# Performance work log

Hardware: AMD Instinct MI355X
Metric: run time of the kernel (lower is better)

Reference implementation:

```python
import jax, jax.numpy as jnp
import numpy as np

B, D, H, W = 8, 512, 96, 96
K1, K2, K3 = 16, 32, 64
EPS = 1e-5


def setup_inputs() -> dict:
    key = jax.random.key(0)
    ks = jax.random.split(key, 20)
    std1 = 1.0 / np.sqrt(K1 * D)
    std2 = 1.0 / np.sqrt(K2 * D)
    std3 = 1.0 / np.sqrt(K3 * D)
    return {
        "X": jax.random.normal(ks[0], (B, D, H, W), jnp.float32),
        "W1": jax.random.normal(ks[1], (D, D), jnp.float32) * 0.02,
        "bn1_scale": jax.random.uniform(ks[2], (D,), jnp.float32, 0.5, 1.5),
        "bn1_bias": jax.random.normal(ks[3], (D,), jnp.float32) * 0.1,
        "bn1_mean": jax.random.normal(ks[4], (D,), jnp.float32) * 0.1,
        "bn1_var": jax.random.uniform(ks[5], (D,), jnp.float32, 0.5, 1.5),
        "W2": jax.random.normal(ks[6], (D, D), jnp.float32) * 0.02,
        "bn2_scale": jax.random.uniform(ks[7], (D,), jnp.float32, 0.5, 1.5),
        "bn2_bias": jax.random.normal(ks[8], (D,), jnp.float32) * 0.1,
        "bn2_mean": jax.random.normal(ks[9], (D,), jnp.float32) * 0.1,
        "bn2_var": jax.random.uniform(ks[10], (D,), jnp.float32, 0.5, 1.5),
        "cw1": jax.random.uniform(ks[11], (D, K1), jnp.float32, -std1, std1),
        "cw2": jax.random.uniform(ks[12], (D, K2), jnp.float32, -std2, std2),
        "cw3": jax.random.uniform(ks[13], (D, K3), jnp.float32, -std3, std3),
        "gamma1": jax.random.normal(ks[14], (1,), jnp.float32) * 0.1,
        "gamma2": jax.random.normal(ks[15], (1,), jnp.float32) * 0.1,
        "gamma3": jax.random.normal(ks[16], (1,), jnp.float32) * 0.1,
    }


def _conv_bn_relu(x, w, s, b, m, v):
    # 1x1 conv (no bias) + eval-mode BatchNorm + ReLU; x: [B,D,H,W], w: [Dout,Din]
    y = jnp.einsum('bdhw,ed->behw', x, w)
    scale = (s / jnp.sqrt(v + EPS))[None, :, None, None]
    shift = (b - m * s / jnp.sqrt(v + EPS))[None, :, None, None]
    return jax.nn.relu(y * scale + shift)


def _soft_vq(x, cw, gamma):
    # x: [B,D,H,W], cw: [D,K] -> gamma * softmax(Xt@cw) @ cw^T, reshaped back
    b, d, h, w = x.shape
    xt = x.reshape(b, d, h * w).transpose(0, 2, 1)          # [B,N,D]
    a = jax.nn.softmax(jnp.einsum('bnd,dk->bnk', xt, cw), axis=-1)
    e = jnp.einsum('bnk,dk->bnd', a, cw)                    # [B,N,D]
    return gamma[0] * e.transpose(0, 2, 1).reshape(b, d, h, w)


def reference(X, W1, bn1_scale, bn1_bias, bn1_mean, bn1_var,
              W2, bn2_scale, bn2_bias, bn2_mean, bn2_var,
              cw1, cw2, cw3, gamma1, gamma2, gamma3):
    X2 = _conv_bn_relu(X, W1, bn1_scale, bn1_bias, bn1_mean, bn1_var)
    X3 = _conv_bn_relu(X2, W2, bn2_scale, bn2_bias, bn2_mean, bn2_var)
    E1 = _soft_vq(X, cw1, gamma1)
    E2 = _soft_vq(X2, cw2, gamma2)
    E3 = _soft_vq(X3, cw3, gamma3)
    return X + E1 + E2 + E3
```

## Files before the change

kernel.cpp:

```cpp
#include <hip/hip_runtime.h>
#include <hip/hip_bf16.h>
#include <stdint.h>

#define DD 512
#define HW 9216
#define NBATCH 8
#define BN_EPS 1e-5f

typedef __attribute__((ext_vector_type(8))) short short8;
typedef __attribute__((ext_vector_type(4))) float f32x4;

__device__ __forceinline__ unsigned short f2bf(float f) {
  union { float f; uint32_t u; } v; v.f = f;
  uint32_t r = v.u + 0x7FFFu + ((v.u >> 16) & 1u);
  return (unsigned short)(r >> 16);
}

__global__ void prep_kernel(const float* __restrict__ W1, const float* __restrict__ W2,
                            const float* __restrict__ s1, const float* __restrict__ b1,
                            const float* __restrict__ m1, const float* __restrict__ v1,
                            const float* __restrict__ s2, const float* __restrict__ b2,
                            const float* __restrict__ m2, const float* __restrict__ v2,
                            unsigned short* __restrict__ W1b, unsigned short* __restrict__ W2b,
                            float* __restrict__ sc1, float* __restrict__ sh1,
                            float* __restrict__ sc2, float* __restrict__ sh2) {
  int t = blockIdx.x * 256 + threadIdx.x;
  if (t < DD * DD) { W1b[t] = f2bf(W1[t]); W2b[t] = f2bf(W2[t]); }
  if (t < DD) {
    float a = s1[t] * rsqrtf(v1[t] + BN_EPS);
    sc1[t] = a; sh1[t] = b1[t] - m1[t] * a;
    float c = s2[t] * rsqrtf(v2[t] + BN_EPS);
    sc2[t] = c; sh2[t] = b2[t] - m2[t] * c;
  }
}

__global__ void prep_cw(const float* __restrict__ cw1, const float* __restrict__ cw2,
                        const float* __restrict__ cw3,
                        unsigned short* __restrict__ CWt, unsigned short* __restrict__ CWc) {
  int t = blockIdx.x * 256 + threadIdx.x;
  int d = t >> 7, k = t & 127;
  float v = 0.f;
  if (k < 16) v = cw1[d * 16 + k];
  else if (k < 48) v = cw2[d * 32 + (k - 16)];
  else if (k < 112) v = cw3[d * 64 + (k - 48)];
  unsigned short bv = f2bf(v);
  CWc[d * 128 + k] = bv;
  if (k < 112) CWt[k * 512 + d] = bv;
}

template <int TIN_BF16>
__global__ __launch_bounds__(256) void gemm_bn(
    const void* __restrict__ Xin_, const unsigned short* __restrict__ Wb,
    const float* __restrict__ scale, const float* __restrict__ shift,
    unsigned short* __restrict__ Yout) {
  const int b  = blockIdx.z;
  const int e0 = blockIdx.y * 128;
  const int n0 = blockIdx.x * 128;
  const int tid  = threadIdx.x;
  const int lane = tid & 63;
  const int wave = tid >> 6;
  const int wr = wave >> 1, wc = wave & 1;

  __shared__ __align__(16) unsigned short Alds[128 * 32];
  __shared__ __align__(16) unsigned short Blds[128 * 40];

  const float* Xf          = (const float*)Xin_ + (size_t)b * DD * HW;
  const unsigned short* Xh = (const unsigned short*)Xin_ + (size_t)b * DD * HW;

  f32x4 acc[4][4];
#pragma unroll
  for (int i = 0; i < 4; i++)
#pragma unroll
    for (int j = 0; j < 4; j++) acc[i][j] = (f32x4)0.0f;

  const int arow  = tid >> 1;
  const int ahalf = tid & 1;
  const int bcol  = tid & 127;
  const int bdh   = tid >> 7;

  const int koff = (lane >> 4) * 8;
  const int lrow = lane & 15;

  for (int kt = 0; kt < DD / 32; ++kt) {
    const int d0 = kt * 32;
    __syncthreads();
    {
      const unsigned short* src = Wb + (size_t)(e0 + arow) * DD + d0 + ahalf * 16;
      short8 v0 = *(const short8*)(src);
      short8 v1 = *(const short8*)(src + 8);
      *(short8*)&Alds[arow * 32 + ahalf * 16]     = v0;
      *(short8*)&Alds[arow * 32 + ahalf * 16 + 8] = v1;
    }
    {
      unsigned short* dst = &Blds[bcol * 40 + bdh * 16];
      if (TIN_BF16) {
        const unsigned short* src = Xh + (size_t)(d0 + bdh * 16) * HW + n0 + bcol;
#pragma unroll
        for (int j = 0; j < 8; j++) {
          uint32_t u0 = src[(size_t)(2 * j) * HW];
          uint32_t u1 = src[(size_t)(2 * j + 1) * HW];
          *(uint32_t*)&dst[2 * j] = u0 | (u1 << 16);
        }
      } else {
        const float* src = Xf + (size_t)(d0 + bdh * 16) * HW + n0 + bcol;
#pragma unroll
        for (int j = 0; j < 8; j++) {
          uint32_t u0 = f2bf(src[(size_t)(2 * j) * HW]);
          uint32_t u1 = f2bf(src[(size_t)(2 * j + 1) * HW]);
          *(uint32_t*)&dst[2 * j] = u0 | (u1 << 16);
        }
      }
    }
    __syncthreads();

    short8 af[4], bfr[4];
#pragma unroll
    for (int ma = 0; ma < 4; ma++)
      af[ma] = *(const short8*)&Alds[(wr * 64 + ma * 16 + lrow) * 32 + koff];
#pragma unroll
    for (int nb = 0; nb < 4; nb++)
      bfr[nb] = *(const short8*)&Blds[(wc * 64 + nb * 16 + lrow) * 40 + koff];
#pragma unroll
    for (int ma = 0; ma < 4; ma++)
#pragma unroll
      for (int nb = 0; nb < 4; nb++)
        acc[ma][nb] = __builtin_amdgcn_mfma_f32_16x16x32_bf16(af[ma], bfr[nb], acc[ma][nb], 0, 0, 0);
  }

  const int rbase = (lane >> 4) * 4;
  const int col   = lane & 15;
#pragma unroll
  for (int ma = 0; ma < 4; ma++) {
    const int ebase = e0 + wr * 64 + ma * 16 + rbase;
    float sc[4], sh[4];
#pragma unroll
    for (int r = 0; r < 4; r++) { sc[r] = scale[ebase + r]; sh[r] = shift[ebase + r]; }
#pragma unroll
    for (int nb = 0; nb < 4; nb++) {
      const int n = n0 + wc * 64 + nb * 16 + col;
      const size_t base = (size_t)b * DD * HW + (size_t)ebase * HW + n;
#pragma unroll
      for (int r = 0; r < 4; r++) {
        float y = acc[ma][nb][r] * sc[r] + sh[r];
        y = y > 0.f ? y : 0.f;
        Yout[base + (size_t)r * HW] = f2bf(y);
      }
    }
  }
}

__global__ __launch_bounds__(256) void vq_mfma(
    const float* __restrict__ X, const unsigned short* __restrict__ X2,
    const unsigned short* __restrict__ X3,
    const unsigned short* __restrict__ CWt,
    const unsigned short* __restrict__ CWc,
    const float* __restrict__ gg1, const float* __restrict__ gg2,
    const float* __restrict__ gg3, float* __restrict__ out) {
  const int b  = blockIdx.y;
  const int n0 = blockIdx.x * 64;
  const int tid  = threadIdx.x;
  const int lane = tid & 63;
  const int wv   = tid >> 6;
  const int hi = lane >> 4, lr = lane & 15;

  __shared__ __align__(16) unsigned short Pl[64 * 136];
  __shared__ __align__(16) unsigned short Stg[17408];

  const size_t bbase = (size_t)b * DD * HW;

  f32x4 accl[7];
#pragma unroll
  for (int t = 0; t < 7; t++) accl[t] = (f32x4)0.0f;

  const int sn = tid & 63;
  const int sg = tid >> 6;

  for (int kt = 0; kt < 16; ++kt) {
    const int d0 = kt * 32;
    __syncthreads();
    {
      const float* src = X + bbase + (size_t)(d0 + sg * 8) * HW + n0 + sn;
      unsigned short* dst = &Stg[sn * 40 + sg * 8];
#pragma unroll
      for (int j = 0; j < 4; j++) {
        uint32_t u0 = f2bf(src[(size_t)(2 * j) * HW]);
        uint32_t u1 = f2bf(src[(size_t)(2 * j + 1) * HW]);
        *(uint32_t*)&dst[2 * j] = u0 | (u1 << 16);
      }
    }
    {
      const unsigned short* src = X2 + bbase + (size_t)(d0 + sg * 8) * HW + n0 + sn;
      unsigned short* dst = &Stg[2560 + sn * 40 + sg * 8];
#pragma unroll
      for (int j = 0; j < 4; j++) {
        uint32_t u0 = src[(size_t)(2 * j) * HW];
        uint32_t u1 = src[(size_t)(2 * j + 1) * HW];
        *(uint32_t*)&dst[2 * j] = u0 | (u1 << 16);
      }
    }
    {
      const unsigned short* src = X3 + bbase + (size_t)(d0 + sg * 8) * HW + n0 + sn;
      unsigned short* dst = &Stg[5120 + sn * 40 + sg * 8];
#pragma unroll
      for (int j = 0; j < 4; j++) {
        uint32_t u0 = src[(size_t)(2 * j) * HW];
        uint32_t u1 = src[(size_t)(2 * j + 1) * HW];
        *(uint32_t*)&dst[2 * j] = u0 | (u1 << 16);
      }
    }
    {
#pragma unroll
      for (int u = tid; u < 1792; u += 256) {
        int row = u >> 4, c = u & 15;
        uint32_t v = *(const uint32_t*)&CWt[row * 512 + d0 + c * 2];
        *(uint32_t*)&Stg[7680 + row * 40 + c * 2] = v;
      }
    }
    __syncthreads();

    short8 a0 = *(const short8*)&Stg[(wv * 16 + lr) * 40 + hi * 8];
    short8 a1 = *(const short8*)&Stg[2560 + (wv * 16 + lr) * 40 + hi * 8];
    short8 a2 = *(const short8*)&Stg[5120 + (wv * 16 + lr) * 40 + hi * 8];
    short8 bt[7];
#pragma unroll
    for (int t = 0; t < 7; t++)
      bt[t] = *(const short8*)&Stg[7680 + (t * 16 + lr) * 40 + hi * 8];
    accl[0] = __builtin_amdgcn_mfma_f32_16x16x32_bf16(a0, bt[0], accl[0], 0, 0, 0);
    accl[1] = __builtin_amdgcn_mfma_f32_16x16x32_bf16(a1, bt[1], accl[1], 0, 0, 0);
    accl[2] = __builtin_amdgcn_mfma_f32_16x16x32_bf16(a1, bt[2], accl[2], 0, 0, 0);
#pragma unroll
    for (int t = 3; t < 7; t++)
      accl[t] = __builtin_amdgcn_mfma_f32_16x16x32_bf16(a2, bt[t], accl[t], 0, 0, 0);
  }

  {
    const float gv1 = gg1[0], gv2 = gg2[0], gv3 = gg3[0];
    float p[7][4];
#pragma unroll
    for (int r = 0; r < 4; ++r) {
      {
        float v = accl[0][r];
        float m = v;
#pragma unroll
        for (int mk = 1; mk <= 8; mk <<= 1) m = fmaxf(m, __shfl_xor(m, mk, 64));
        float e = __expf(v - m);
        float s = e;
#pragma unroll
        for (int mk = 1; mk <= 8; mk <<= 1) s += __shfl_xor(s, mk, 64);
        p[0][r] = e * (gv1 / s);
      }
      {
        float v1 = accl[1][r], v2 = accl[2][r];
        float m = fmaxf(v1, v2);
#pragma unroll
        for (int mk = 1; mk <= 8; mk <<= 1) m = fmaxf(m, __shfl_xor(m, mk, 64));
        float e1 = __expf(v1 - m), e2 = __expf(v2 - m);
        float s = e1 + e2;
#pragma unroll
        for (int mk = 1; mk <= 8; mk <<= 1) s += __shfl_xor(s, mk, 64);
        float sc = gv2 / s;
        p[1][r] = e1 * sc; p[2][r] = e2 * sc;
      }
      {
        float m = fmaxf(fmaxf(accl[3][r], accl[4][r]), fmaxf(accl[5][r], accl[6][r]));
#pragma unroll
        for (int mk = 1; mk <= 8; mk <<= 1) m = fmaxf(m, __shfl_xor(m, mk, 64));
        float e[4], s = 0.f;
#pragma unroll
        for (int t = 0; t < 4; t++) { e[t] = __expf(accl[3 + t][r] - m); s += e[t]; }
#pragma unroll
        for (int mk = 1; mk <= 8; mk <<= 1) s += __shfl_xor(s, mk, 64);
        float sc = gv3 / s;
#pragma unroll
        for (int t = 0; t < 4; t++) p[3 + t][r] = e[t] * sc;
      }
    }
    const int posr = wv * 16 + 4 * hi;
#pragma unroll
    for (int t = 0; t < 7; ++t)
#pragma unroll
      for (int r = 0; r < 4; ++r)
        Pl[(posr + r) * 136 + t * 16 + lr] = f2bf(p[t][r]);
    {
      int pp = tid & 63, cg = tid >> 6;
#pragma unroll
      for (int i = 0; i < 4; ++i) Pl[pp * 136 + 112 + cg * 4 + i] = 0;
    }
  }
  __syncthreads();

  short8 pf[4][4];
#pragma unroll
  for (int ct = 0; ct < 4; ++ct)
#pragma unroll
    for (int s = 0; s < 4; ++s)
      pf[ct][s] = *(const short8*)&Pl[(ct * 16 + lr) * 136 + s * 32 + hi * 8];

  const float* Xg = X + bbase;
  float* outg = out + bbase;
  for (int chunk = 0; chunk < 4; ++chunk) {
    __syncthreads();
    {
      int row = tid >> 1, half = tid & 1;
      const unsigned short* src = CWc + (size_t)(chunk * 128 + row) * 128 + half * 64;
      unsigned short* dst = &Stg[row * 136 + half * 64];
#pragma unroll
      for (int i = 0; i < 8; ++i)
        *(short8*)(dst + i * 8) = *(const short8*)(src + i * 8);
    }
    __syncthreads();
#pragma unroll
    for (int dl = wv; dl < 8; dl += 4) {
      f32x4 acc[4];
#pragma unroll
      for (int ct = 0; ct < 4; ++ct) acc[ct] = (f32x4)0.0f;
#pragma unroll
      for (int s = 0; s < 4; ++s) {
        short8 af = *(const short8*)&Stg[(dl * 16 + lr) * 136 + s * 32 + hi * 8];
#pragma unroll
        for (int ct = 0; ct < 4; ++ct)
          acc[ct] = __builtin_amdgcn_mfma_f32_16x16x32_bf16(af, pf[ct][s], acc[ct], 0, 0, 0);
      }
      const int dgb = chunk * 128 + dl * 16 + 4 * hi;
#pragma unroll
      for (int ct = 0; ct < 4; ++ct) {
        const int n = n0 + ct * 16 + lr;
#pragma unroll
        for (int r = 0; r < 4; ++r) {
          const size_t a = (size_t)(dgb + r) * HW + n;
          outg[a] = Xg[a] + acc[ct][r];
        }
      }
    }
  }
}

extern "C" void kernel_launch(void* const* d_in, const int* in_sizes, int n_in,
                              void* d_out, int out_size, void* d_ws, size_t ws_size,
                              hipStream_t stream) {
  const float* X    = (const float*)d_in[0];
  const float* W1   = (const float*)d_in[1];
  const float* bn1s = (const float*)d_in[2];
  const float* bn1b = (const float*)d_in[3];
  const float* bn1m = (const float*)d_in[4];
  const float* bn1v = (const float*)d_in[5];
  const float* W2   = (const float*)d_in[6];
  const float* bn2s = (const float*)d_in[7];
  const float* bn2b = (const float*)d_in[8];
  const float* bn2m = (const float*)d_in[9];
  const float* bn2v = (const float*)d_in[10];
  const float* cw1  = (const float*)d_in[11];
  const float* cw2  = (const float*)d_in[12];
  const float* cw3  = (const float*)d_in[13];
  const float* g1   = (const float*)d_in[14];
  const float* g2   = (const float*)d_in[15];
  const float* g3   = (const float*)d_in[16];

  char* ws = (char*)d_ws;
  unsigned short* W1b = (unsigned short*)(ws);
  unsigned short* W2b = (unsigned short*)(ws + 524288);
  float* sc1 = (float*)(ws + 1048576);
  float* sh1 = sc1 + 512;
  float* sc2 = sh1 + 512;
  float* sh2 = sc2 + 512;
  unsigned short* CWt = (unsigned short*)(ws + 1064960);
  unsigned short* CWc = (unsigned short*)(ws + 1064960 + 114688);
  unsigned short* X2 = (unsigned short*)(ws + (1 << 21));
  unsigned short* X3 = X2 + (size_t)NBATCH * DD * HW;

  prep_kernel<<<1024, 256, 0, stream>>>(W1, W2, bn1s, bn1b, bn1m, bn1v,
                                        bn2s, bn2b, bn2m, bn2v,
                                        W1b, W2b, sc1, sh1, sc2, sh2);
  prep_cw<<<256, 256, 0, stream>>>(cw1, cw2, cw3, CWt, CWc);

  dim3 gg(HW / 128, DD / 128, NBATCH);
  gemm_bn<0><<<gg, 256, 0, stream>>>((const void*)X,  W1b, sc1, sh1, X2);
  gemm_bn<1><<<gg, 256, 0, stream>>>((const void*)X2, W2b, sc2, sh2, X3);

  dim3 gv(HW / 64, NBATCH);
  vq_mfma<<<gv, 256, 0, stream>>>(X, X2, X3, CWt, CWc, g1, g2, g3, (float*)d_out);
}
```

Baseline: 329.5 us.

## Load VQ operands directly into MFMA registers, drop LDS staging and barriers

The VQ kernel no longer stages X/X2/X3 tiles and codewords through shared memory with two barriers per k-step. Each lane now loads its MFMA operand fragments straight from global memory, with the operand roles swapped so the softmax reduction works along the register dimension and needs fewer cross-lane shuffles. The output projection also reads codewords directly from global memory instead of copying chunks into LDS. This removes synchronisation and LDS traffic, at the cost of more redundant global/L2 reads of the codewords by every wave.

```diff
diff --git a/kernel.cpp b/kernel.cpp
--- a/kernel.cpp
+++ b/kernel.cpp
@@ -9,6 +9,8 @@
 
 typedef __attribute__((ext_vector_type(8))) short short8;
 typedef __attribute__((ext_vector_type(4))) float f32x4;
+
+union bf8u { uint32_t u[4]; short8 v; };
 
 __device__ __forceinline__ unsigned short f2bf(float f) {
   union { float f; uint32_t u; } v; v.f = f;
@@ -164,127 +166,117 @@
   const int hi = lane >> 4, lr = lane & 15;
 
   __shared__ __align__(16) unsigned short Pl[64 * 136];
-  __shared__ __align__(16) unsigned short Stg[17408];
 
   const size_t bbase = (size_t)b * DD * HW;
+  const int myn = n0 + wv * 16 + lr;
+  const float*          pX  = X  + bbase + myn;
+  const unsigned short* pX2 = X2 + bbase + myn;
+  const unsigned short* pX3 = X3 + bbase + myn;
 
   f32x4 accl[7];
 #pragma unroll
   for (int t = 0; t < 7; t++) accl[t] = (f32x4)0.0f;
-
-  const int sn = tid & 63;
-  const int sg = tid >> 6;
 
   for (int kt = 0; kt < 16; ++kt) {
     const int d0 = kt * 32;
-    __syncthreads();
-    {
-      const float* src = X + bbase + (size_t)(d0 + sg * 8) * HW + n0 + sn;
-      unsigned short* dst = &Stg[sn * 40 + sg * 8];
-#pragma unroll
-      for (int j = 0; j < 4; j++) {
-        uint32_t u0 = f2bf(src[(size_t)(2 * j) * HW]);
-        uint32_t u1 = f2bf(src[(size_t)(2 * j + 1) * HW]);
-        *(uint32_t*)&dst[2 * j] = u0 | (u1 << 16);
-      }
-    }
-    {
-      const unsigned short* src = X2 + bbase + (size_t)(d0 + sg * 8) * HW + n0 + sn;
-      unsigned short* dst = &Stg[2560 + sn * 40 + sg * 8];
-#pragma unroll
-      for (int j = 0; j < 4; j++) {
-        uint32_t u0 = src[(size_t)(2 * j) * HW];
-        uint32_t u1 = src[(size_t)(2 * j + 1) * HW];
-        *(uint32_t*)&dst[2 * j] = u0 | (u1 << 16);
-      }
-    }
-    {
-      const unsigned short* src = X3 + bbase + (size_t)(d0 + sg * 8) * HW + n0 + sn;
-      unsigned short* dst = &Stg[5120 + sn * 40 + sg * 8];
-#pragma unroll
-      for (int j = 0; j < 4; j++) {
-        uint32_t u0 = src[(size_t)(2 * j) * HW];
-        uint32_t u1 = src[(size_t)(2 * j + 1) * HW];
-        *(uint32_t*)&dst[2 * j] = u0 | (u1 << 16);
-      }
-    }
-    {
-#pragma unroll
-      for (int u = tid; u < 1792; u += 256) {
-        int row = u >> 4, c = u & 15;
-        uint32_t v = *(const uint32_t*)&CWt[row * 512 + d0 + c * 2];
-        *(uint32_t*)&Stg[7680 + row * 40 + c * 2] = v;
-      }
-    }
-    __syncthreads();
-
-    short8 a0 = *(const short8*)&Stg[(wv * 16 + lr) * 40 + hi * 8];
-    short8 a1 = *(const short8*)&Stg[2560 + (wv * 16 + lr) * 40 + hi * 8];
-    short8 a2 = *(const short8*)&Stg[5120 + (wv * 16 + lr) * 40 + hi * 8];
-    short8 bt[7];
+    const size_t rbase = (size_t)(d0 + hi * 8) * HW;
+
+    bf8u bx, b2, b3;
+#pragma unroll
+    for (int j = 0; j < 4; j++) {
+      uint32_t u0 = f2bf(pX[rbase + (size_t)(2 * j) * HW]);
+      uint32_t u1 = f2bf(pX[rbase + (size_t)(2 * j + 1) * HW]);
+      bx.u[j] = u0 | (u1 << 16);
+    }
+#pragma unroll
+    for (int j = 0; j < 4; j++) {
+      uint32_t u0 = pX2[rbase + (size_t)(2 * j) * HW];
+      uint32_t u1 = pX2[rbase + (size_t)(2 * j + 1) * HW];
+      b2.u[j] = u0 | (u1 << 16);
+    }
+#pragma unroll
+    for (int j = 0; j < 4; j++) {
+      uint32_t u0 = pX3[rbase + (size_t)(2 * j) * HW];
+      uint32_t u1 = pX3[rbase + (size_t)(2 * j + 1) * HW];
+      b3.u[j] = u0 | (u1 << 16);
+    }
+
+    short8 at[7];
 #pragma unroll
     for (int t = 0; t < 7; t++)
-      bt[t] = *(const short8*)&Stg[7680 + (t * 16 + lr) * 40 + hi * 8];
-    accl[0] = __builtin_amdgcn_mfma_f32_16x16x32_bf16(a0, bt[0], accl[0], 0, 0, 0);
-    accl[1] = __builtin_amdgcn_mfma_f32_16x16x32_bf16(a1, bt[1], accl[1], 0, 0, 0);
-    accl[2] = __builtin_amdgcn_mfma_f32_16x16x32_bf16(a1, bt[2], accl[2], 0, 0, 0);
+      at[t] = *(const short8*)&CWt[(size_t)(t * 16 + lr) * 512 + d0 + hi * 8];
+
+    accl[0] = __builtin_amdgcn_mfma_f32_16x16x32_bf16(at[0], bx.v, accl[0], 0, 0, 0);
+    accl[1] = __builtin_amdgcn_mfma_f32_16x16x32_bf16(at[1], b2.v, accl[1], 0, 0, 0);
+    accl[2] = __builtin_amdgcn_mfma_f32_16x16x32_bf16(at[2], b2.v, accl[2], 0, 0, 0);
 #pragma unroll
     for (int t = 3; t < 7; t++)
-      accl[t] = __builtin_amdgcn_mfma_f32_16x16x32_bf16(a2, bt[t], accl[t], 0, 0, 0);
+      accl[t] = __builtin_amdgcn_mfma_f32_16x16x32_bf16(at[t], b3.v, accl[t], 0, 0, 0);
   }
 
   {
     const float gv1 = gg1[0], gv2 = gg2[0], gv3 = gg3[0];
-    float p[7][4];
-#pragma unroll
-    for (int r = 0; r < 4; ++r) {
-      {
-        float v = accl[0][r];
-        float m = v;
-#pragma unroll
-        for (int mk = 1; mk <= 8; mk <<= 1) m = fmaxf(m, __shfl_xor(m, mk, 64));
-        float e = __expf(v - m);
-        float s = e;
-#pragma unroll
-        for (int mk = 1; mk <= 8; mk <<= 1) s += __shfl_xor(s, mk, 64);
-        p[0][r] = e * (gv1 / s);
+    const int prow = (wv * 16 + lr) * 136;
+    {
+      float m = fmaxf(fmaxf(accl[0][0], accl[0][1]), fmaxf(accl[0][2], accl[0][3]));
+      m = fmaxf(m, __shfl_xor(m, 16, 64));
+      m = fmaxf(m, __shfl_xor(m, 32, 64));
+      float e[4], s = 0.f;
+#pragma unroll
+      for (int r = 0; r < 4; r++) { e[r] = __expf(accl[0][r] - m); s += e[r]; }
+      s += __shfl_xor(s, 16, 64);
+      s += __shfl_xor(s, 32, 64);
+      float sc = gv1 / s;
+#pragma unroll
+      for (int r = 0; r < 4; r++) Pl[prow + 4 * hi + r] = f2bf(e[r] * sc);
+    }
+    {
+      float m = accl[1][0];
+#pragma unroll
+      for (int r = 1; r < 4; r++) m = fmaxf(m, accl[1][r]);
+#pragma unroll
+      for (int r = 0; r < 4; r++) m = fmaxf(m, accl[2][r]);
+      m = fmaxf(m, __shfl_xor(m, 16, 64));
+      m = fmaxf(m, __shfl_xor(m, 32, 64));
+      float e1[4], e2[4], s = 0.f;
+#pragma unroll
+      for (int r = 0; r < 4; r++) { e1[r] = __expf(accl[1][r] - m); s += e1[r]; }
+#pragma unroll
+      for (int r = 0; r < 4; r++) { e2[r] = __expf(accl[2][r] - m); s += e2[r]; }
+      s += __shfl_xor(s, 16, 64);
+      s += __shfl_xor(s, 32, 64);
+      float sc = gv2 / s;
+#pragma unroll
+      for (int r = 0; r < 4; r++) {
+        Pl[prow + 16 + 4 * hi + r] = f2bf(e1[r] * sc);
+        Pl[prow + 32 + 4 * hi + r] = f2bf(e2[r] * sc);
       }
-      {
-        float v1 = accl[1][r], v2 = accl[2][r];
-        float m = fmaxf(v1, v2);
-#pragma unroll
-        for (int mk = 1; mk <= 8; mk <<= 1) m = fmaxf(m, __shfl_xor(m, mk, 64));
-        float e1 = __expf(v1 - m), e2 = __expf(v2 - m);
-        float s = e1 + e2;
-#pragma unroll
-        for (int mk = 1; mk <= 8; mk <<= 1) s += __shfl_xor(s, mk, 64);
-        float sc = gv2 / s;
-        p[1][r] = e1 * sc; p[2][r] = e2 * sc;
-      }
-      {
-        float m = fmaxf(fmaxf(accl[3][r], accl[4][r]), fmaxf(accl[5][r], accl[6][r]));
-#pragma unroll
-        for (int mk = 1; mk <= 8; mk <<= 1) m = fmaxf(m, __shfl_xor(m, mk, 64));
-        float e[4], s = 0.f;
-#pragma unroll
-        for (int t = 0; t < 4; t++) { e[t] = __expf(accl[3 + t][r] - m); s += e[t]; }
-#pragma unroll
-        for (int mk = 1; mk <= 8; mk <<= 1) s += __shfl_xor(s, mk, 64);
-        float sc = gv3 / s;
-#pragma unroll
-        for (int t = 0; t < 4; t++) p[3 + t][r] = e[t] * sc;
-      }
-    }
-    const int posr = wv * 16 + 4 * hi;
-#pragma unroll
-    for (int t = 0; t < 7; ++t)
-#pragma unroll
-      for (int r = 0; r < 4; ++r)
-        Pl[(posr + r) * 136 + t * 16 + lr] = f2bf(p[t][r]);
+    }
+    {
+      float m = accl[3][0];
+#pragma unroll
+      for (int t = 3; t < 7; t++)
+#pragma unroll
+        for (int r = 0; r < 4; r++) m = fmaxf(m, accl[t][r]);
+      m = fmaxf(m, __shfl_xor(m, 16, 64));
+      m = fmaxf(m, __shfl_xor(m, 32, 64));
+      float e[4][4], s = 0.f;
+#pragma unroll
+      for (int t = 0; t < 4; t++)
+#pragma unroll
+        for (int r = 0; r < 4; r++) { e[t][r] = __expf(accl[3 + t][r] - m); s += e[t][r]; }
+      s += __shfl_xor(s, 16, 64);
+      s += __shfl_xor(s, 32, 64);
+      float sc = gv3 / s;
+#pragma unroll
+      for (int t = 0; t < 4; t++)
+#pragma unroll
+        for (int r = 0; r < 4; r++)
+          Pl[prow + 48 + 16 * t + 4 * hi + r] = f2bf(e[t][r] * sc);
+    }
     {
       int pp = tid & 63, cg = tid >> 6;
-#pragma unroll
-      for (int i = 0; i < 4; ++i) Pl[pp * 136 + 112 + cg * 4 + i] = 0;
+      *(uint64_t*)&Pl[pp * 136 + 112 + cg * 4] = 0;
     }
   }
   __syncthreads();
@@ -298,38 +290,26 @@
 
   const float* Xg = X + bbase;
   float* outg = out + bbase;
-  for (int chunk = 0; chunk < 4; ++chunk) {
-    __syncthreads();
-    {
-      int row = tid >> 1, half = tid & 1;
-      const unsigned short* src = CWc + (size_t)(chunk * 128 + row) * 128 + half * 64;
-      unsigned short* dst = &Stg[row * 136 + half * 64];
-#pragma unroll
-      for (int i = 0; i < 8; ++i)
-        *(short8*)(dst + i * 8) = *(const short8*)(src + i * 8);
-    }
-    __syncthreads();
-#pragma unroll
-    for (int dl = wv; dl < 8; dl += 4) {
-      f32x4 acc[4];
-#pragma unroll
-      for (int ct = 0; ct < 4; ++ct) acc[ct] = (f32x4)0.0f;
-#pragma unroll
-      for (int s = 0; s < 4; ++s) {
-        short8 af = *(const short8*)&Stg[(dl * 16 + lr) * 136 + s * 32 + hi * 8];
-#pragma unroll
-        for (int ct = 0; ct < 4; ++ct)
-          acc[ct] = __builtin_amdgcn_mfma_f32_16x16x32_bf16(af, pf[ct][s], acc[ct], 0, 0, 0);
-      }
-      const int dgb = chunk * 128 + dl * 16 + 4 * hi;
-#pragma unroll
-      for (int ct = 0; ct < 4; ++ct) {
-        const int n = n0 + ct * 16 + lr;
-#pragma unroll
-        for (int r = 0; r < 4; ++r) {
-          const size_t a = (size_t)(dgb + r) * HW + n;
-          outg[a] = Xg[a] + acc[ct][r];
-        }
+#pragma unroll 2
+  for (int dt = wv; dt < 32; dt += 4) {
+    f32x4 acc3[4];
+#pragma unroll
+    for (int ct = 0; ct < 4; ++ct) acc3[ct] = (f32x4)0.0f;
+#pragma unroll
+    for (int s = 0; s < 4; ++s) {
+      short8 af = *(const short8*)&CWc[(size_t)(dt * 16 + lr) * 128 + s * 32 + hi * 8];
+#pragma unroll
+      for (int ct = 0; ct < 4; ++ct)
+        acc3[ct] = __builtin_amdgcn_mfma_f32_16x16x32_bf16(af, pf[ct][s], acc3[ct], 0, 0, 0);
+    }
+    const int dgb = dt * 16 + 4 * hi;
+#pragma unroll
+    for (int ct = 0; ct < 4; ++ct) {
+      const int n = n0 + ct * 16 + lr;
+#pragma unroll
+      for (int r = 0; r < 4; ++r) {
+        const size_t a = (size_t)(dgb + r) * HW + n;
+        outg[a] = Xg[a] + acc3[ct][r];
       }
     }
   }
```

After: 536.4 us. 62.8% more time.
